# Optimization experiments

Hardware: AMD Instinct MI355X
Metric: run time of the kernel (lower is better)

The kernel has to match this reference:

```python
import jax, jax.numpy as jnp
import numpy as np

N, R, D, K = 2048, 64, 64, 512  # batch, n_roles, filler_embed_dim, n_fillers
LAMBDA_VQ, LAMBDA_COMMIT, LAMBDA_ORTH = 1.0, 0.5, 0.0


def setup_inputs() -> dict:
    key = jax.random.key(0)
    k1, k2 = jax.random.split(key)
    soft_fillers = jax.random.normal(k1, (N, R, D), dtype=jnp.float32)
    weight = jax.random.normal(k2, (K, D), dtype=jnp.float32)  # codebook rows
    return {"soft_fillers": soft_fillers, "weight": weight}


def _nearest(x, w):
    # x: [M, D], w: [K, D] -> nearest codebook rows + indices
    d = (jnp.sum(x * x, axis=-1, keepdims=True)
         - 2.0 * (x @ w.T)
         + jnp.sum(w * w, axis=-1))          # [M, K]
    idx = jnp.argmin(d, axis=-1)              # [M]
    return w[idx], idx                        # gather: [M, D]


def reference(soft_fillers, weight):
    flat = soft_fillers.reshape(-1, D)        # [N*R, D]

    # Path 1: weight_sg=True -> weight detached, straight-through to input
    q_sg_flat, idx = _nearest(flat, jax.lax.stop_gradient(weight))
    q_sg_flat = flat + jax.lax.stop_gradient(q_sg_flat - flat)

    # Path 2: input detached -> gradient flows to weight via gather
    q_flat, _ = _nearest(jax.lax.stop_gradient(flat), weight)

    q_sg = q_sg_flat.reshape(N, R, D)
    q = q_flat.reshape(N, R, D)
    filler_idxs = idx.reshape(N, R)

    # vq loss: mean over (N, D) of L2-norm over roles of elementwise-squared diff
    t_vq = (q - jax.lax.stop_gradient(soft_fillers)) ** 2          # [N, R, D]
    vq_loss = jnp.mean(jnp.sqrt(jnp.sum(t_vq * t_vq, axis=1)))
    t_c = (jax.lax.stop_gradient(q) - soft_fillers) ** 2
    commit_loss = jnp.mean(jnp.sqrt(jnp.sum(t_c * t_c, axis=1)))

    # semi-orthogonality penalty on weight.t() (rows of codebook): ||W^T W - I||_F
    gram = weight.T @ weight                                        # [D, D]
    orth_penalty = jnp.linalg.norm(gram - jnp.eye(D, dtype=weight.dtype))

    total_loss = (LAMBDA_VQ * vq_loss + LAMBDA_COMMIT * commit_loss
                  + LAMBDA_ORTH * orth_penalty)

    filler_rank = jnp.linalg.matrix_rank(weight).astype(jnp.float32)

    return (total_loss, vq_loss, commit_loss, orth_penalty, filler_rank,
            q_sg, q, filler_idxs)
```

## Files before the change

kernel.cpp:

```cpp
#include <hip/hip_runtime.h>
#include <math.h>

#define N_ 2048
#define R_ 64
#define D_ 64
#define K_ 512
#define M_ (N_*R_)
#define BM 128
#define TAU 0.05f
#define CHK 0.02f

#define WN_OFF   16
#define GRAM_OFF 1024
#define WBF_BYTE 32768
#define WS_NEED  163840

typedef __attribute__((ext_vector_type(8))) short s16x8;
typedef __attribute__((ext_vector_type(4))) float f32x4;

static __device__ __forceinline__ unsigned short f2bf(float f) {
    unsigned u = __float_as_uint(f);
    u += 0x7FFFu + ((u >> 16) & 1u);
    return (unsigned short)(u >> 16);
}
static __device__ __forceinline__ float bf2f(unsigned short h) {
    return __uint_as_float(((unsigned)h) << 16);
}

static __device__ __forceinline__ int xs_byte(int r, int q) {
    return r * 256 + (q >> 3) * 128 + (((q & 7) ^ (r & 7)) * 16);
}

__global__ void k_pre(const float* __restrict__ w, float* __restrict__ ws, int pre) {
    const int b = blockIdx.x, t = threadIdx.x;
    if (b < 64) {
        __shared__ float red[4][64];
        const int i = b, j = t & 63, kg = t >> 6;
        float s = 0.f;
        for (int k = kg * 128; k < kg * 128 + 128; ++k)
            s = fmaf(w[k * 64 + i], w[k * 64 + j], s);
        red[kg][j] = s;
        __syncthreads();
        if (t < 64)
            ws[GRAM_OFF + i * 64 + t] = red[0][t] + red[1][t] + red[2][t] + red[3][t];
    } else if (b < 66) {
        const int code = (b - 64) * 256 + t;
        const float4* wr = (const float4*)(w + code * 64);
        float s = 0.f;
#pragma unroll
        for (int i = 0; i < 16; ++i) {
            float4 v = wr[i];
            s += v.x * v.x + v.y * v.y + v.z * v.z + v.w * v.w;
        }
        ws[WN_OFF + code] = s;
        if (b == 64 && t == 0) ws[0] = 0.f;
    } else {
        if (!pre) return;
        const int code = (b - 66) * 256 + t;
        char* whi = (char*)ws + WBF_BYTE;
        char* wlo = whi + 65536;
        const int c = code >> 6, rr = code & 63;
        const int nt = rr >> 4, lr = rr & 15;
        for (int kg = 0; kg < 8; ++kg) {
            float4 v0 = *(const float4*)(w + code * 64 + kg * 8);
            float4 v1 = *(const float4*)(w + code * 64 + kg * 8 + 4);
            const float vv[8] = {v0.x, v0.y, v0.z, v0.w, v1.x, v1.y, v1.z, v1.w};
            s16x8 ph, pl;
#pragma unroll
            for (int j = 0; j < 8; ++j) {
                const unsigned short hb = f2bf(vv[j]);
                ph[j] = (short)hb;
                pl[j] = (short)f2bf(vv[j] - bf2f(hb));
            }
            const int s = kg >> 2, g = kg & 3, l = g * 16 + lr;
            const int off = (((c * 2 + s) * 4 + nt) << 10) + l * 16;
            *(s16x8*)(whi + off) = ph;
            *(s16x8*)(wlo + off) = pl;
        }
    }
}

template<bool PRE>
__global__ __launch_bounds__(256, 4) void k_argmin(
    const float* __restrict__ x, const float* __restrict__ w,
    float* __restrict__ ws, float* __restrict__ out)
{
    __shared__ __align__(16) float xs[BM * 64];
    __shared__ float sb1[BM];
    __shared__ float sb2[BM];
    __shared__ int   ridx[BM];
    __shared__ int   ulist[BM];
    __shared__ int   nunc;

    const int t = threadIdx.x;
    const int l = t & 63, wid = t >> 6;
    const int g = l >> 4, lr = l & 15;
    const long base = (long)blockIdx.x * BM;
    const float* wn_g = ws + WN_OFF;
    const char* whi = (const char*)ws + WBF_BYTE;
    const char* wlo = whi + 65536;

    if (t == 0) nunc = 0;

#pragma unroll
    for (int it = 0; it < 8; ++it) {
        const int idx = it * 256 + t;
        const int r = idx >> 4, q = idx & 15;
        const float4 v = *(const float4*)(x + (base + r) * 64 + q * 4);
        *(float4*)((char*)xs + xs_byte(r, q)) = v;
    }
    __syncthreads();

    s16x8 ah[2][2], al[2][2];
#pragma unroll
    for (int mt = 0; mt < 2; ++mt) {
        const int row = wid * 32 + mt * 16 + lr;
#pragma unroll
        for (int s = 0; s < 2; ++s) {
            const int kg = s * 4 + g;
            const float4 v0 = *(const float4*)((const char*)xs + xs_byte(row, kg * 2));
            const float4 v1 = *(const float4*)((const char*)xs + xs_byte(row, kg * 2 + 1));
            const float vv[8] = {v0.x, v0.y, v0.z, v0.w, v1.x, v1.y, v1.z, v1.w};
            s16x8 ph, pl;
#pragma unroll
            for (int j = 0; j < 8; ++j) {
                const unsigned short hb = f2bf(vv[j]);
                ph[j] = (short)hb;
                pl[j] = (short)f2bf(vv[j] - bf2f(hb));
            }
            ah[mt][s] = ph; al[mt][s] = pl;
        }
    }

    float b1[2][4], b2[2][4]; int i1[2][4];
#pragma unroll
    for (int mt = 0; mt < 2; ++mt)
#pragma unroll
        for (int j = 0; j < 4; ++j) { b1[mt][j] = 3.4e38f; b2[mt][j] = 3.4e38f; i1[mt][j] = 0; }

    for (int c = 0; c < 8; ++c) {
        const int cbase = c * 64;
        f32x4 acc[2][4];
        const f32x4 z = {0.f, 0.f, 0.f, 0.f};
#pragma unroll
        for (int mt = 0; mt < 2; ++mt)
#pragma unroll
            for (int nt = 0; nt < 4; ++nt) acc[mt][nt] = z;

#pragma unroll
        for (int s = 0; s < 2; ++s) {
            s16x8 bh[4], bl[4];
#pragma unroll
            for (int nt = 0; nt < 4; ++nt) {
                if constexpr (PRE) {
                    const int off = (((c * 2 + s) * 4 + nt) << 10) + l * 16;
                    bh[nt] = *(const s16x8*)(whi + off);
                    bl[nt] = *(const s16x8*)(wlo + off);
                } else {
                    const int crow = cbase + nt * 16 + lr;
                    const float* src = w + (long)crow * 64 + (s * 4 + g) * 8;
                    const float4 v0 = *(const float4*)src;
                    const float4 v1 = *(const float4*)(src + 4);
                    const float vv[8] = {v0.x, v0.y, v0.z, v0.w, v1.x, v1.y, v1.z, v1.w};
                    s16x8 ph, pl;
#pragma unroll
                    for (int j = 0; j < 8; ++j) {
                        const unsigned short hb = f2bf(vv[j]);
                        ph[j] = (short)hb;
                        pl[j] = (short)f2bf(vv[j] - bf2f(hb));
                    }
                    bh[nt] = ph; bl[nt] = pl;
                }
            }
#pragma unroll
            for (int nt = 0; nt < 4; ++nt)
#pragma unroll
                for (int mt = 0; mt < 2; ++mt) {
                    acc[mt][nt] = __builtin_amdgcn_mfma_f32_16x16x32_bf16(ah[mt][s], bh[nt], acc[mt][nt], 0, 0, 0);
                    acc[mt][nt] = __builtin_amdgcn_mfma_f32_16x16x32_bf16(al[mt][s], bh[nt], acc[mt][nt], 0, 0, 0);
                    acc[mt][nt] = __builtin_amdgcn_mfma_f32_16x16x32_bf16(ah[mt][s], bl[nt], acc[mt][nt], 0, 0, 0);
                }
        }

#pragma unroll
        for (int nt = 0; nt < 4; ++nt) {
            const int code = cbase + nt * 16 + lr;
            const float wnv = wn_g[code];
#pragma unroll
            for (int mt = 0; mt < 2; ++mt)
#pragma unroll
                for (int j = 0; j < 4; ++j) {
                    const float sv = fmaf(-2.f, acc[mt][nt][j], wnv);
                    if (sv < b1[mt][j]) { b2[mt][j] = b1[mt][j]; b1[mt][j] = sv; i1[mt][j] = code; }
                    else if (sv < b2[mt][j]) b2[mt][j] = sv;
                }
        }
    }

    float g1[2][4]; int gi1[2][4];
#pragma unroll
    for (int mt = 0; mt < 2; ++mt)
#pragma unroll
        for (int j = 0; j < 4; ++j) { g1[mt][j] = b1[mt][j]; gi1[mt][j] = i1[mt][j]; }
#pragma unroll
    for (int m = 1; m < 16; m <<= 1) {
#pragma unroll
        for (int mt = 0; mt < 2; ++mt)
#pragma unroll
            for (int j = 0; j < 4; ++j) {
                const float ov = __shfl_xor(g1[mt][j], m, 64);
                const int   oi = __shfl_xor(gi1[mt][j], m, 64);
                if (ov < g1[mt][j] || (ov == g1[mt][j] && oi < gi1[mt][j])) {
                    g1[mt][j] = ov; gi1[mt][j] = oi;
                }
            }
    }
    float g2[2][4];
#pragma unroll
    for (int mt = 0; mt < 2; ++mt)
#pragma unroll
        for (int j = 0; j < 4; ++j)
            g2[mt][j] = (i1[mt][j] == gi1[mt][j]) ? b2[mt][j] : b1[mt][j];
#pragma unroll
    for (int m = 1; m < 16; m <<= 1) {
#pragma unroll
        for (int mt = 0; mt < 2; ++mt)
#pragma unroll
            for (int j = 0; j < 4; ++j)
                g2[mt][j] = fminf(g2[mt][j], __shfl_xor(g2[mt][j], m, 64));
    }

    if (lr == 0) {
#pragma unroll
        for (int mt = 0; mt < 2; ++mt)
#pragma unroll
            for (int j = 0; j < 4; ++j) {
                const int rl = wid * 32 + mt * 16 + g * 4 + j;
                ridx[rl] = gi1[mt][j];
                sb1[rl] = g1[mt][j];
                sb2[rl] = g2[mt][j];
            }
    }
    __syncthreads();

    if (t < BM) {
        const int ci = ridx[t];
        const float* wrow = w + (long)ci * 64;
        float dot = 0.f;
#pragma unroll
        for (int p = 0; p < 16; ++p) {
            const float4 xv = *(const float4*)((const char*)xs + xs_byte(t, p));
            const float4 wv = *(const float4*)(wrow + p * 4);
            dot = fmaf(xv.x, wv.x, dot);
            dot = fmaf(xv.y, wv.y, dot);
            dot = fmaf(xv.z, wv.z, dot);
            dot = fmaf(xv.w, wv.w, dot);
        }
        const float sex = fmaf(-2.f, dot, wn_g[ci]);
        const bool unc = ((sb2[t] - sb1[t]) < TAU) || (fabsf(sex - sb1[t]) > CHK);
        if (unc) { const int p = atomicAdd(&nunc, 1); ulist[p] = t; }
    }
    __syncthreads();

    const int nu = nunc;
    if (nu > 0) {
        for (int e = wid; e < nu; e += 4) {
            const int r = ulist[e];
            float bv = 3.4e38f; int bi = 0;
            for (int cc = 0; cc < 8; ++cc) {
                const int code = cc * 64 + l;
                const float* wrow = w + (long)code * 64;
                float dot = 0.f;
#pragma unroll
                for (int p = 0; p < 16; ++p) {
                    const float4 xv = *(const float4*)((const char*)xs + xs_byte(r, p));
                    const float4 wv = *(const float4*)(wrow + p * 4);
                    dot = fmaf(xv.x, wv.x, dot);
                    dot = fmaf(xv.y, wv.y, dot);
                    dot = fmaf(xv.z, wv.z, dot);
                    dot = fmaf(xv.w, wv.w, dot);
                }
                const float sv = fmaf(-2.f, dot, wn_g[code]);
                if (sv < bv) { bv = sv; bi = code; }
            }
#pragma unroll
            for (int m = 1; m < 64; m <<= 1) {
                const float ov = __shfl_xor(bv, m, 64);
                const int   oi = __shfl_xor(bi, m, 64);
                if (ov < bv || (ov == bv && oi < bi)) { bv = ov; bi = oi; }
            }
            if (l == 0) ridx[r] = bi;
        }
    }
    __syncthreads();

    float* q_sg = out + 5;
    float* q    = out + 5 + (long)M_ * 64;
    float* fidx = out + 5 + 2L * M_ * 64;
    const int ry = t >> 4, dq = t & 15;
    float4 va = {0.f, 0.f, 0.f, 0.f}, vb = {0.f, 0.f, 0.f, 0.f};
#pragma unroll
    for (int i = 0; i < 8; ++i) {
        const int r = i * 16 + ry;
        const float4 wv = *(const float4*)(w + (long)ridx[r] * 64 + dq * 4);
        const float4 xv = *(const float4*)((const char*)xs + xs_byte(r, dq));
        const long off = (base + r) * 64 + dq * 4;
        *(float4*)(q_sg + off) = wv;
        *(float4*)(q + off) = wv;
        float4 p;
        p.x = (wv.x - xv.x) * (wv.x - xv.x);
        p.y = (wv.y - xv.y) * (wv.y - xv.y);
        p.z = (wv.z - xv.z) * (wv.z - xv.z);
        p.w = (wv.w - xv.w) * (wv.w - xv.w);
        if (i < 4) {
            va.x = fmaf(p.x, p.x, va.x); va.y = fmaf(p.y, p.y, va.y);
            va.z = fmaf(p.z, p.z, va.z); va.w = fmaf(p.w, p.w, va.w);
        } else {
            vb.x = fmaf(p.x, p.x, vb.x); vb.y = fmaf(p.y, p.y, vb.y);
            vb.z = fmaf(p.z, p.z, vb.z); vb.w = fmaf(p.w, p.w, vb.w);
        }
    }
    if (t < BM) fidx[base + t] = (float)ridx[t];
    __syncthreads();
    float* red = xs;
    *(float4*)(red + ((0 * 16 + ry) * 16 + dq) * 4) = va;
    *(float4*)(red + ((1 * 16 + ry) * 16 + dq) * 4) = vb;
    __syncthreads();
    if (t < 128) {
        const int n = t >> 6, dcol = t & 63;
        float s = 0.f;
#pragma unroll
        for (int u = 0; u < 16; ++u)
            s += red[((n * 16 + u) * 16 + (dcol >> 2)) * 4 + (dcol & 3)];
        float v = sqrtf(s);
#pragma unroll
        for (int m = 1; m < 64; m <<= 1) v += __shfl_xor(v, m, 64);
        if (dcol == 0) atomicAdd(ws + 0, v);
    }
}

__global__ void k_final(const float* __restrict__ ws, float* __restrict__ out)
{
    __shared__ float g[64][65];
    __shared__ float osum[4];
    __shared__ float tol;
    const int t = threadIdx.x;
    float oacc = 0.f;
    for (int i = t; i < 4096; i += 256) {
        const int r = i >> 6, cl = i & 63;
        const float gv = ws[GRAM_OFF + i];
        g[r][cl] = gv;
        const float p = gv - (r == cl ? 1.f : 0.f);
        oacc = fmaf(p, p, oacc);
    }
#pragma unroll
    for (int m = 1; m < 64; m <<= 1) oacc += __shfl_xor(oacc, m, 64);
    if ((t & 63) == 0) osum[t >> 6] = oacc;
    __syncthreads();

    if (t == 0) {
        float maxd = 0.f;
        for (int i = 0; i < 64; ++i) maxd = fmaxf(maxd, fabsf(g[i][i]));
        tol = maxd * 1e-7f + 1e-30f;
    }
    __syncthreads();

    int rank = 0;
    const int j = t & 63, rq = t >> 6;
    for (int s = 0; s < 64; ++s) {
        const float p = g[s][s];
        const bool ok = fabsf(p) > tol;
        if (ok) {
            rank++;
            if (j > s) {
                const float rp = 1.f / p;
                const float gsj = g[s][j];
                for (int r = s + 1 + rq; r < 64; r += 4)
                    g[r][j] = fmaf(-(g[r][s] * rp), gsj, g[r][j]);
            }
        }
        __syncthreads();
    }

    if (t == 0) {
        const float vq = ws[0] / (float)(N_ * D_);
        const float orth = sqrtf(osum[0] + osum[1] + osum[2] + osum[3]);
        out[0] = 1.5f * vq;
        out[1] = vq;
        out[2] = vq;
        out[3] = orth;
        out[4] = (float)rank;
    }
}

extern "C" void kernel_launch(void* const* d_in, const int* in_sizes, int n_in,
                              void* d_out, int out_size, void* d_ws, size_t ws_size,
                              hipStream_t stream) {
    const float* x = (const float*)d_in[0];
    const float* w = (const float*)d_in[1];
    float* out = (float*)d_out;
    float* ws  = (float*)d_ws;
    const int pre = (ws_size >= (size_t)WS_NEED) ? 1 : 0;

    hipLaunchKernelGGL(k_pre, dim3(68), dim3(256), 0, stream, w, ws, pre);
    if (pre)
        hipLaunchKernelGGL((k_argmin<true>),  dim3(M_/BM), dim3(256), 0, stream, x, w, ws, out);
    else
        hipLaunchKernelGGL((k_argmin<false>), dim3(M_/BM), dim3(256), 0, stream, x, w, ws, out);
    hipLaunchKernelGGL(k_final, dim3(1), dim3(256), 0, stream, ws, out);
}
```

Before: 168.5 us.

## Keep codebook split in registers per wave and loop persistent blocks over row tiles

The argmin kernel now runs 256 persistent blocks of 512 threads. Each of the 8 waves holds a 64-code slice of the bf16 hi/lo split codebook in registers for the whole kernel, and the block loops over 8 tiles of 64 rows. This removes the per-block reloading of codebook fragments and the separate precomputed bf16 workspace, at the cost of a cross-wave shared-memory argmin merge and more synchronisation per tile. The vq-loss reduction is reworked to go through a shared buffer, with one atomic per block.

```diff
diff --git a/kernel.cpp b/kernel.cpp
--- a/kernel.cpp
+++ b/kernel.cpp
@@ -6,14 +6,11 @@
 #define D_ 64
 #define K_ 512
 #define M_ (N_*R_)
-#define BM 128
 #define TAU 0.05f
 #define CHK 0.02f
 
 #define WN_OFF   16
 #define GRAM_OFF 1024
-#define WBF_BYTE 32768
-#define WS_NEED  163840
 
 typedef __attribute__((ext_vector_type(8))) short s16x8;
 typedef __attribute__((ext_vector_type(4))) float f32x4;
@@ -31,7 +28,16 @@
     return r * 256 + (q >> 3) * 128 + (((q & 7) ^ (r & 7)) * 16);
 }
 
-__global__ void k_pre(const float* __restrict__ w, float* __restrict__ ws, int pre) {
+static __device__ __forceinline__ void split8(const float* vv, s16x8& ph, s16x8& pl) {
+#pragma unroll
+    for (int j = 0; j < 8; ++j) {
+        const unsigned short hb = f2bf(vv[j]);
+        ph[j] = (short)hb;
+        pl[j] = (short)f2bf(vv[j] - bf2f(hb));
+    }
+}
+
+__global__ void k_pre(const float* __restrict__ w, float* __restrict__ ws) {
     const int b = blockIdx.x, t = threadIdx.x;
     if (b < 64) {
         __shared__ float red[4][64];
@@ -43,7 +49,7 @@
         __syncthreads();
         if (t < 64)
             ws[GRAM_OFF + i * 64 + t] = red[0][t] + red[1][t] + red[2][t] + red[3][t];
-    } else if (b < 66) {
+    } else {
         const int code = (b - 64) * 256 + t;
         const float4* wr = (const float4*)(w + code * 64);
         float s = 0.f;
@@ -54,289 +60,223 @@
         }
         ws[WN_OFF + code] = s;
         if (b == 64 && t == 0) ws[0] = 0.f;
-    } else {
-        if (!pre) return;
-        const int code = (b - 66) * 256 + t;
-        char* whi = (char*)ws + WBF_BYTE;
-        char* wlo = whi + 65536;
-        const int c = code >> 6, rr = code & 63;
-        const int nt = rr >> 4, lr = rr & 15;
-        for (int kg = 0; kg < 8; ++kg) {
-            float4 v0 = *(const float4*)(w + code * 64 + kg * 8);
-            float4 v1 = *(const float4*)(w + code * 64 + kg * 8 + 4);
-            const float vv[8] = {v0.x, v0.y, v0.z, v0.w, v1.x, v1.y, v1.z, v1.w};
-            s16x8 ph, pl;
-#pragma unroll
-            for (int j = 0; j < 8; ++j) {
-                const unsigned short hb = f2bf(vv[j]);
-                ph[j] = (short)hb;
-                pl[j] = (short)f2bf(vv[j] - bf2f(hb));
-            }
-            const int s = kg >> 2, g = kg & 3, l = g * 16 + lr;
-            const int off = (((c * 2 + s) * 4 + nt) << 10) + l * 16;
-            *(s16x8*)(whi + off) = ph;
-            *(s16x8*)(wlo + off) = pl;
-        }
-    }
-}
-
-template<bool PRE>
-__global__ __launch_bounds__(256, 4) void k_argmin(
+    }
+}
+
+__global__ __launch_bounds__(512, 2) void k_argmin(
     const float* __restrict__ x, const float* __restrict__ w,
     float* __restrict__ ws, float* __restrict__ out)
 {
-    __shared__ __align__(16) float xs[BM * 64];
-    __shared__ float sb1[BM];
-    __shared__ float sb2[BM];
-    __shared__ int   ridx[BM];
-    __shared__ int   ulist[BM];
+    __shared__ __align__(16) float xs[4096];
+    __shared__ __align__(16) float dbuf[4096];
+    __shared__ float mb1[8][64], mb2[8][64];
+    __shared__ int   mi_[8][64];
+    __shared__ float fb1[64], fb2[64];
+    __shared__ int   ridx[64];
+    __shared__ int   ulist[64];
     __shared__ int   nunc;
 
     const int t = threadIdx.x;
     const int l = t & 63, wid = t >> 6;
     const int g = l >> 4, lr = l & 15;
-    const long base = (long)blockIdx.x * BM;
+    const long brow = (long)blockIdx.x * 512;
     const float* wn_g = ws + WN_OFF;
-    const char* whi = (const char*)ws + WBF_BYTE;
-    const char* wlo = whi + 65536;
-
-    if (t == 0) nunc = 0;
-
-#pragma unroll
-    for (int it = 0; it < 8; ++it) {
-        const int idx = it * 256 + t;
-        const int r = idx >> 4, q = idx & 15;
-        const float4 v = *(const float4*)(x + (base + r) * 64 + q * 4);
-        *(float4*)((char*)xs + xs_byte(r, q)) = v;
-    }
-    __syncthreads();
-
-    s16x8 ah[2][2], al[2][2];
-#pragma unroll
-    for (int mt = 0; mt < 2; ++mt) {
-        const int row = wid * 32 + mt * 16 + lr;
-#pragma unroll
-        for (int s = 0; s < 2; ++s) {
-            const int kg = s * 4 + g;
-            const float4 v0 = *(const float4*)((const char*)xs + xs_byte(row, kg * 2));
-            const float4 v1 = *(const float4*)((const char*)xs + xs_byte(row, kg * 2 + 1));
-            const float vv[8] = {v0.x, v0.y, v0.z, v0.w, v1.x, v1.y, v1.z, v1.w};
-            s16x8 ph, pl;
-#pragma unroll
-            for (int j = 0; j < 8; ++j) {
-                const unsigned short hb = f2bf(vv[j]);
-                ph[j] = (short)hb;
-                pl[j] = (short)f2bf(vv[j] - bf2f(hb));
-            }
-            ah[mt][s] = ph; al[mt][s] = pl;
-        }
-    }
-
-    float b1[2][4], b2[2][4]; int i1[2][4];
-#pragma unroll
-    for (int mt = 0; mt < 2; ++mt)
-#pragma unroll
-        for (int j = 0; j < 4; ++j) { b1[mt][j] = 3.4e38f; b2[mt][j] = 3.4e38f; i1[mt][j] = 0; }
-
-    for (int c = 0; c < 8; ++c) {
-        const int cbase = c * 64;
-        f32x4 acc[2][4];
-        const f32x4 z = {0.f, 0.f, 0.f, 0.f};
-#pragma unroll
-        for (int mt = 0; mt < 2; ++mt)
-#pragma unroll
-            for (int nt = 0; nt < 4; ++nt) acc[mt][nt] = z;
-
-#pragma unroll
-        for (int s = 0; s < 2; ++s) {
-            s16x8 bh[4], bl[4];
-#pragma unroll
-            for (int nt = 0; nt < 4; ++nt) {
-                if constexpr (PRE) {
-                    const int off = (((c * 2 + s) * 4 + nt) << 10) + l * 16;
-                    bh[nt] = *(const s16x8*)(whi + off);
-                    bl[nt] = *(const s16x8*)(wlo + off);
-                } else {
-                    const int crow = cbase + nt * 16 + lr;
-                    const float* src = w + (long)crow * 64 + (s * 4 + g) * 8;
-                    const float4 v0 = *(const float4*)src;
-                    const float4 v1 = *(const float4*)(src + 4);
-                    const float vv[8] = {v0.x, v0.y, v0.z, v0.w, v1.x, v1.y, v1.z, v1.w};
-                    s16x8 ph, pl;
-#pragma unroll
-                    for (int j = 0; j < 8; ++j) {
-                        const unsigned short hb = f2bf(vv[j]);
-                        ph[j] = (short)hb;
-                        pl[j] = (short)f2bf(vv[j] - bf2f(hb));
-                    }
-                    bh[nt] = ph; bl[nt] = pl;
-                }
-            }
-#pragma unroll
-            for (int nt = 0; nt < 4; ++nt)
-#pragma unroll
-                for (int mt = 0; mt < 2; ++mt) {
-                    acc[mt][nt] = __builtin_amdgcn_mfma_f32_16x16x32_bf16(ah[mt][s], bh[nt], acc[mt][nt], 0, 0, 0);
-                    acc[mt][nt] = __builtin_amdgcn_mfma_f32_16x16x32_bf16(al[mt][s], bh[nt], acc[mt][nt], 0, 0, 0);
-                    acc[mt][nt] = __builtin_amdgcn_mfma_f32_16x16x32_bf16(ah[mt][s], bl[nt], acc[mt][nt], 0, 0, 0);
-                }
-        }
-
-#pragma unroll
-        for (int nt = 0; nt < 4; ++nt) {
-            const int code = cbase + nt * 16 + lr;
-            const float wnv = wn_g[code];
-#pragma unroll
-            for (int mt = 0; mt < 2; ++mt)
-#pragma unroll
-                for (int j = 0; j < 4; ++j) {
-                    const float sv = fmaf(-2.f, acc[mt][nt][j], wnv);
-                    if (sv < b1[mt][j]) { b2[mt][j] = b1[mt][j]; b1[mt][j] = sv; i1[mt][j] = code; }
-                    else if (sv < b2[mt][j]) b2[mt][j] = sv;
-                }
-        }
-    }
-
-    float g1[2][4]; int gi1[2][4];
-#pragma unroll
-    for (int mt = 0; mt < 2; ++mt)
-#pragma unroll
-        for (int j = 0; j < 4; ++j) { g1[mt][j] = b1[mt][j]; gi1[mt][j] = i1[mt][j]; }
-#pragma unroll
-    for (int m = 1; m < 16; m <<= 1) {
-#pragma unroll
-        for (int mt = 0; mt < 2; ++mt)
-#pragma unroll
-            for (int j = 0; j < 4; ++j) {
-                const float ov = __shfl_xor(g1[mt][j], m, 64);
-                const int   oi = __shfl_xor(gi1[mt][j], m, 64);
-                if (ov < g1[mt][j] || (ov == g1[mt][j] && oi < gi1[mt][j])) {
-                    g1[mt][j] = ov; gi1[mt][j] = oi;
-                }
-            }
-    }
-    float g2[2][4];
-#pragma unroll
-    for (int mt = 0; mt < 2; ++mt)
-#pragma unroll
-        for (int j = 0; j < 4; ++j)
-            g2[mt][j] = (i1[mt][j] == gi1[mt][j]) ? b2[mt][j] : b1[mt][j];
-#pragma unroll
-    for (int m = 1; m < 16; m <<= 1) {
-#pragma unroll
-        for (int mt = 0; mt < 2; ++mt)
-#pragma unroll
-            for (int j = 0; j < 4; ++j)
-                g2[mt][j] = fminf(g2[mt][j], __shfl_xor(g2[mt][j], m, 64));
-    }
-
-    if (lr == 0) {
-#pragma unroll
-        for (int mt = 0; mt < 2; ++mt)
-#pragma unroll
-            for (int j = 0; j < 4; ++j) {
-                const int rl = wid * 32 + mt * 16 + g * 4 + j;
-                ridx[rl] = gi1[mt][j];
-                sb1[rl] = g1[mt][j];
-                sb2[rl] = g2[mt][j];
-            }
-    }
-    __syncthreads();
-
-    if (t < BM) {
-        const int ci = ridx[t];
-        const float* wrow = w + (long)ci * 64;
-        float dot = 0.f;
-#pragma unroll
-        for (int p = 0; p < 16; ++p) {
-            const float4 xv = *(const float4*)((const char*)xs + xs_byte(t, p));
-            const float4 wv = *(const float4*)(wrow + p * 4);
-            dot = fmaf(xv.x, wv.x, dot);
-            dot = fmaf(xv.y, wv.y, dot);
-            dot = fmaf(xv.z, wv.z, dot);
-            dot = fmaf(xv.w, wv.w, dot);
-        }
-        const float sex = fmaf(-2.f, dot, wn_g[ci]);
-        const bool unc = ((sb2[t] - sb1[t]) < TAU) || (fabsf(sex - sb1[t]) > CHK);
-        if (unc) { const int p = atomicAdd(&nunc, 1); ulist[p] = t; }
-    }
-    __syncthreads();
-
-    const int nu = nunc;
-    if (nu > 0) {
-        for (int e = wid; e < nu; e += 4) {
-            const int r = ulist[e];
-            float bv = 3.4e38f; int bi = 0;
-            for (int cc = 0; cc < 8; ++cc) {
-                const int code = cc * 64 + l;
-                const float* wrow = w + (long)code * 64;
-                float dot = 0.f;
-#pragma unroll
-                for (int p = 0; p < 16; ++p) {
-                    const float4 xv = *(const float4*)((const char*)xs + xs_byte(r, p));
-                    const float4 wv = *(const float4*)(wrow + p * 4);
-                    dot = fmaf(xv.x, wv.x, dot);
-                    dot = fmaf(xv.y, wv.y, dot);
-                    dot = fmaf(xv.z, wv.z, dot);
-                    dot = fmaf(xv.w, wv.w, dot);
-                }
-                const float sv = fmaf(-2.f, dot, wn_g[code]);
-                if (sv < bv) { bv = sv; bi = code; }
-            }
-#pragma unroll
-            for (int m = 1; m < 64; m <<= 1) {
-                const float ov = __shfl_xor(bv, m, 64);
-                const int   oi = __shfl_xor(bi, m, 64);
-                if (ov < bv || (ov == bv && oi < bi)) { bv = ov; bi = oi; }
-            }
-            if (l == 0) ridx[r] = bi;
-        }
-    }
-    __syncthreads();
 
     float* q_sg = out + 5;
     float* q    = out + 5 + (long)M_ * 64;
     float* fidx = out + 5 + 2L * M_ * 64;
-    const int ry = t >> 4, dq = t & 15;
-    float4 va = {0.f, 0.f, 0.f, 0.f}, vb = {0.f, 0.f, 0.f, 0.f};
-#pragma unroll
-    for (int i = 0; i < 8; ++i) {
-        const int r = i * 16 + ry;
-        const float4 wv = *(const float4*)(w + (long)ridx[r] * 64 + dq * 4);
-        const float4 xv = *(const float4*)((const char*)xs + xs_byte(r, dq));
-        const long off = (base + r) * 64 + dq * 4;
-        *(float4*)(q_sg + off) = wv;
-        *(float4*)(q + off) = wv;
-        float4 p;
-        p.x = (wv.x - xv.x) * (wv.x - xv.x);
-        p.y = (wv.y - xv.y) * (wv.y - xv.y);
-        p.z = (wv.z - xv.z) * (wv.z - xv.z);
-        p.w = (wv.w - xv.w) * (wv.w - xv.w);
-        if (i < 4) {
-            va.x = fmaf(p.x, p.x, va.x); va.y = fmaf(p.y, p.y, va.y);
-            va.z = fmaf(p.z, p.z, va.z); va.w = fmaf(p.w, p.w, va.w);
-        } else {
-            vb.x = fmaf(p.x, p.x, vb.x); vb.y = fmaf(p.y, p.y, vb.y);
-            vb.z = fmaf(p.z, p.z, vb.z); vb.w = fmaf(p.w, p.w, vb.w);
-        }
-    }
-    if (t < BM) fidx[base + t] = (float)ridx[t];
-    __syncthreads();
-    float* red = xs;
-    *(float4*)(red + ((0 * 16 + ry) * 16 + dq) * 4) = va;
-    *(float4*)(red + ((1 * 16 + ry) * 16 + dq) * 4) = vb;
-    __syncthreads();
-    if (t < 128) {
-        const int n = t >> 6, dcol = t & 63;
-        float s = 0.f;
-#pragma unroll
-        for (int u = 0; u < 16; ++u)
-            s += red[((n * 16 + u) * 16 + (dcol >> 2)) * 4 + (dcol & 3)];
-        float v = sqrtf(s);
-#pragma unroll
-        for (int m = 1; m < 64; m <<= 1) v += __shfl_xor(v, m, 64);
-        if (dcol == 0) atomicAdd(ws + 0, v);
-    }
+
+    s16x8 bh[2][4], bl[2][4];
+    float wnv[4];
+#pragma unroll
+    for (int s = 0; s < 2; ++s)
+#pragma unroll
+        for (int nt = 0; nt < 4; ++nt) {
+            const int code = wid * 64 + nt * 16 + lr;
+            const float* src = w + (long)code * 64 + s * 32 + g * 8;
+            const float4 v0 = *(const float4*)src;
+            const float4 v1 = *(const float4*)(src + 4);
+            const float vv[8] = {v0.x, v0.y, v0.z, v0.w, v1.x, v1.y, v1.z, v1.w};
+            split8(vv, bh[s][nt], bl[s][nt]);
+        }
+#pragma unroll
+    for (int nt = 0; nt < 4; ++nt)
+        wnv[nt] = wn_g[wid * 64 + nt * 16 + lr];
+
+    float vq_acc = 0.f;
+
+    for (int it = 0; it < 8; ++it) {
+        const long rbase = brow + it * 64;
+        if (t == 0) nunc = 0;
+
+#pragma unroll
+        for (int ii = 0; ii < 2; ++ii) {
+            const int gid = ii * 512 + t;
+            const int r = gid >> 4, qq = gid & 15;
+            const float4 v = *(const float4*)(x + (rbase + r) * 64 + qq * 4);
+            *(float4*)((char*)xs + xs_byte(r, qq)) = v;
+        }
+        __syncthreads();
+
+#pragma unroll
+        for (int mt = 0; mt < 4; ++mt) {
+            const int row = mt * 16 + lr;
+            s16x8 ah[2], al[2];
+#pragma unroll
+            for (int s = 0; s < 2; ++s) {
+                const int kg = s * 4 + g;
+                const float4 v0 = *(const float4*)((const char*)xs + xs_byte(row, kg * 2));
+                const float4 v1 = *(const float4*)((const char*)xs + xs_byte(row, kg * 2 + 1));
+                const float vv[8] = {v0.x, v0.y, v0.z, v0.w, v1.x, v1.y, v1.z, v1.w};
+                split8(vv, ah[s], al[s]);
+            }
+            f32x4 acc[4];
+            const f32x4 z = {0.f, 0.f, 0.f, 0.f};
+#pragma unroll
+            for (int nt = 0; nt < 4; ++nt) acc[nt] = z;
+#pragma unroll
+            for (int s = 0; s < 2; ++s)
+#pragma unroll
+                for (int nt = 0; nt < 4; ++nt) {
+                    acc[nt] = __builtin_amdgcn_mfma_f32_16x16x32_bf16(ah[s], bh[s][nt], acc[nt], 0, 0, 0);
+                    acc[nt] = __builtin_amdgcn_mfma_f32_16x16x32_bf16(al[s], bh[s][nt], acc[nt], 0, 0, 0);
+                    acc[nt] = __builtin_amdgcn_mfma_f32_16x16x32_bf16(ah[s], bl[s][nt], acc[nt], 0, 0, 0);
+                }
+
+            float b1[4], b2[4]; int i1[4];
+#pragma unroll
+            for (int j = 0; j < 4; ++j) { b1[j] = 3.4e38f; b2[j] = 3.4e38f; i1[j] = 0; }
+#pragma unroll
+            for (int nt = 0; nt < 4; ++nt) {
+                const int code = wid * 64 + nt * 16 + lr;
+#pragma unroll
+                for (int j = 0; j < 4; ++j) {
+                    const float sv = fmaf(-2.f, acc[nt][j], wnv[nt]);
+                    if (sv < b1[j]) { b2[j] = b1[j]; b1[j] = sv; i1[j] = code; }
+                    else if (sv < b2[j]) b2[j] = sv;
+                }
+            }
+#pragma unroll
+            for (int m = 1; m < 16; m <<= 1) {
+#pragma unroll
+                for (int j = 0; j < 4; ++j) {
+                    const float ov1 = __shfl_xor(b1[j], m, 64);
+                    const int   oi1 = __shfl_xor(i1[j], m, 64);
+                    const float ov2 = __shfl_xor(b2[j], m, 64);
+                    const float nb2 = fminf(fminf(b2[j], ov2), fmaxf(b1[j], ov1));
+                    if (ov1 < b1[j] || (ov1 == b1[j] && oi1 < i1[j])) { b1[j] = ov1; i1[j] = oi1; }
+                    b2[j] = nb2;
+                }
+            }
+            if (lr == 0) {
+#pragma unroll
+                for (int j = 0; j < 4; ++j) {
+                    const int ro = mt * 16 + g * 4 + j;
+                    mb1[wid][ro] = b1[j]; mb2[wid][ro] = b2[j]; mi_[wid][ro] = i1[j];
+                }
+            }
+        }
+        __syncthreads();
+
+        if (t < 64) {
+            float B1 = 3.4e38f, B2 = 3.4e38f; int I = 0;
+#pragma unroll
+            for (int wv = 0; wv < 8; ++wv) {
+                const float a1 = mb1[wv][t], a2 = mb2[wv][t];
+                const int   ai = mi_[wv][t];
+                const float nb2 = fminf(fminf(B2, a2), fmaxf(B1, a1));
+                if (a1 < B1) { B1 = a1; I = ai; }
+                B2 = nb2;
+            }
+            fb1[t] = B1; fb2[t] = B2; ridx[t] = I;
+        }
+        __syncthreads();
+
+        {
+            const int r = t >> 3, sub = t & 7;
+            const int ci = ridx[r];
+            const float4 xa = *(const float4*)((const char*)xs + xs_byte(r, sub * 2));
+            const float4 xb = *(const float4*)((const char*)xs + xs_byte(r, sub * 2 + 1));
+            const float4 wa = *(const float4*)(w + (long)ci * 64 + sub * 8);
+            const float4 wb = *(const float4*)(w + (long)ci * 64 + sub * 8 + 4);
+            float dot = xa.x * wa.x + xa.y * wa.y + xa.z * wa.z + xa.w * wa.w
+                      + xb.x * wb.x + xb.y * wb.y + xb.z * wb.z + xb.w * wb.w;
+            dot += __shfl_down(dot, 4, 8);
+            dot += __shfl_down(dot, 2, 8);
+            dot += __shfl_down(dot, 1, 8);
+            if (sub == 0) {
+                const float sex = fmaf(-2.f, dot, wn_g[ci]);
+                const bool unc = ((fb2[r] - fb1[r]) < TAU) || (fabsf(sex - fb1[r]) > CHK);
+                if (unc) { const int p = atomicAdd(&nunc, 1); ulist[p] = r; }
+            }
+        }
+        __syncthreads();
+
+        const int nu = nunc;
+        if (nu > 0) {
+            for (int e = wid; e < nu; e += 8) {
+                const int r = ulist[e];
+                float bv = 3.4e38f; int bi = 0;
+                for (int cc = 0; cc < 8; ++cc) {
+                    const int code = cc * 64 + l;
+                    const float* wrow = w + (long)code * 64;
+                    float dot = 0.f;
+#pragma unroll
+                    for (int p = 0; p < 16; ++p) {
+                        const float4 xv = *(const float4*)((const char*)xs + xs_byte(r, p));
+                        const float4 wv = *(const float4*)(wrow + p * 4);
+                        dot = fmaf(xv.x, wv.x, dot);
+                        dot = fmaf(xv.y, wv.y, dot);
+                        dot = fmaf(xv.z, wv.z, dot);
+                        dot = fmaf(xv.w, wv.w, dot);
+                    }
+                    const float sv = fmaf(-2.f, dot, wn_g[code]);
+                    if (sv < bv) { bv = sv; bi = code; }
+                }
+#pragma unroll
+                for (int m = 1; m < 64; m <<= 1) {
+                    const float ov = __shfl_xor(bv, m, 64);
+                    const int   oi = __shfl_xor(bi, m, 64);
+                    if (ov < bv || (ov == bv && oi < bi)) { bv = ov; bi = oi; }
+                }
+                if (l == 0) ridx[r] = bi;
+            }
+        }
+        __syncthreads();
+
+#pragma unroll
+        for (int ii = 0; ii < 2; ++ii) {
+            const int gid = ii * 512 + t;
+            const int r = gid >> 4, qq = gid & 15;
+            const int ci = ridx[r];
+            const float4 wv4 = *(const float4*)(w + (long)ci * 64 + qq * 4);
+            const float4 xv4 = *(const float4*)((const char*)xs + xs_byte(r, qq));
+            const long off = (rbase + r) * 64 + qq * 4;
+            *(float4*)(q_sg + off) = wv4;
+            *(float4*)(q + off) = wv4;
+            float4 p;
+            p.x = (wv4.x - xv4.x) * (wv4.x - xv4.x);
+            p.y = (wv4.y - xv4.y) * (wv4.y - xv4.y);
+            p.z = (wv4.z - xv4.z) * (wv4.z - xv4.z);
+            p.w = (wv4.w - xv4.w) * (wv4.w - xv4.w);
+            float4 p2;
+            p2.x = p.x * p.x; p2.y = p.y * p.y; p2.z = p.z * p.z; p2.w = p.w * p.w;
+            *(float4*)(dbuf + r * 64 + qq * 4) = p2;
+        }
+        if (t < 64) fidx[rbase + t] = (float)ridx[t];
+        __syncthreads();
+
+        if (t < 64) {
+            float s = 0.f;
+            for (int r2 = 0; r2 < 64; ++r2) s += dbuf[r2 * 64 + t];
+            float v = sqrtf(s);
+#pragma unroll
+            for (int m = 1; m < 64; m <<= 1) v += __shfl_xor(v, m, 64);
+            if (t == 0) vq_acc += v;
+        }
+        __syncthreads();
+    }
+    if (t == 0) atomicAdd(ws + 0, vq_acc);
 }
 
 __global__ void k_final(const float* __restrict__ ws, float* __restrict__ out)
@@ -400,12 +340,8 @@
     const float* w = (const float*)d_in[1];
     float* out = (float*)d_out;
     float* ws  = (float*)d_ws;
-    const int pre = (ws_size >= (size_t)WS_NEED) ? 1 : 0;
-
-    hipLaunchKernelGGL(k_pre, dim3(68), dim3(256), 0, stream, w, ws, pre);
-    if (pre)
-        hipLaunchKernelGGL((k_argmin<true>),  dim3(M_/BM), dim3(256), 0, stream, x, w, ws, out);
-    else
-        hipLaunchKernelGGL((k_argmin<false>), dim3(M_/BM), dim3(256), 0, stream, x, w, ws, out);
-    hipLaunchKernelGGL(k_final, dim3(1), dim3(256), 0, stream, ws, out);
-}
+
+    hipLaunchKernelGGL(k_pre,    dim3(66),  dim3(256), 0, stream, w, ws);
+    hipLaunchKernelGGL(k_argmin, dim3(256), dim3(512), 0, stream, x, w, ws, out);
+    hipLaunchKernelGGL(k_final,  dim3(1),   dim3(256), 0, stream, ws, out);
+}
```

New measurement: 251.4 us. +49.2%, slower.
